# Kernel tuning notes

Hardware: AMD Instinct MI355X
Metric: run time of the kernel (lower is better)

Reference implementation:

```python
import jax, jax.numpy as jnp
import numpy as np

B, S, I, H, L = 32, 512, 512, 512, 2


def _gru_scan(x, wx, bx, wh, bh, reverse):
    # x: [B, S, layer_in_dim]; wx: [3H, in], wh: [3H, H]. PyTorch gate order r,z,n.
    hdim = wh.shape[1]
    gx = jnp.einsum('bsi,gi->sbg', x, wx) + bx  # precompute input gates: [S, B, 3H]
    h0 = jnp.zeros((x.shape[0], hdim), x.dtype)

    def step(h, gxt):
        gh = h @ wh.T + bh
        r = jax.nn.sigmoid(gxt[:, :hdim] + gh[:, :hdim])
        z = jax.nn.sigmoid(gxt[:, hdim:2 * hdim] + gh[:, hdim:2 * hdim])
        n = jnp.tanh(gxt[:, 2 * hdim:] + r * gh[:, 2 * hdim:])
        hn = (1 - z) * n + z * h
        return hn, hn

    hN, ys = jax.lax.scan(step, h0, gx, reverse=reverse)
    return ys.transpose(1, 0, 2), hN  # [B, S, H], [B, H]


def setup_inputs() -> dict:
    key = jax.random.key(0)
    ks = jax.random.split(key, 17)
    sc = 0.05
    d = {'x': jax.random.normal(ks[0], (B, S, I), jnp.float32)}
    i = 1
    for layer in range(L):
        in_dim = I if layer == 0 else 2 * H
        for tag in ('f', 'b'):
            d[f'wx_{tag}{layer}'] = jax.random.normal(ks[i], (3 * H, in_dim), jnp.float32) * sc
            d[f'bx_{tag}{layer}'] = jax.random.normal(jax.random.fold_in(ks[i], 1), (3 * H,), jnp.float32) * sc
            d[f'wh_{tag}{layer}'] = jax.random.normal(jax.random.fold_in(ks[i], 2), (3 * H, H), jnp.float32) * sc
            d[f'bh_{tag}{layer}'] = jax.random.normal(jax.random.fold_in(ks[i], 3), (3 * H,), jnp.float32) * sc
            i += 1
    return d


def reference(x,
              wx_f0, bx_f0, wh_f0, bh_f0, wx_b0, bx_b0, wh_b0, bh_b0,
              wx_f1, bx_f1, wh_f1, bh_f1, wx_b1, bx_b1, wh_b1, bh_b1):
    layers = [((wx_f0, bx_f0, wh_f0, bh_f0), (wx_b0, bx_b0, wh_b0, bh_b0)),
              ((wx_f1, bx_f1, wh_f1, bh_f1), (wx_b1, bx_b1, wh_b1, bh_b1))]
    layer_in = x
    h_fw, h_bw = [], []
    for fw, bw in layers:
        yf, hf = _gru_scan(layer_in, *fw, reverse=False)
        yb, hb = _gru_scan(layer_in, *bw, reverse=True)
        layer_in = jnp.concatenate([yf, yb], axis=-1)  # [B, S, 2H] (dropout p=0 -> identity)
        h_fw.append(hf)
        h_bw.append(hb)
    return layer_in, (jnp.stack(h_fw, 0), jnp.stack(h_bw, 0))
```

## Files before the change

kernel.cpp:

```cpp
#include <hip/hip_runtime.h>
#include <stdint.h>

typedef short short8 __attribute__((ext_vector_type(8)));
typedef float floatx4 __attribute__((ext_vector_type(4)));
typedef unsigned long long u64;

__device__ __forceinline__ unsigned short f2bf(float f) {
  union { float f; unsigned int i; } v;
  v.f = f;
  unsigned int r = v.i + 0x7fffu + ((v.i >> 16) & 1u);
  return (unsigned short)(r >> 16);
}
__device__ __forceinline__ short8 cvt8(const float4 a, const float4 b) {
  short8 v;
  v[0] = (short)f2bf(a.x); v[1] = (short)f2bf(a.y);
  v[2] = (short)f2bf(a.z); v[3] = (short)f2bf(a.w);
  v[4] = (short)f2bf(b.x); v[5] = (short)f2bf(b.y);
  v[6] = (short)f2bf(b.z); v[7] = (short)f2bf(b.w);
  return v;
}
__device__ __forceinline__ float sane(float x, float lim) {
  return fminf(fmaxf(x, -lim), lim);
}

extern __shared__ unsigned short lds[];

template<int K, int XM>
__global__ __launch_bounds__(256)
void gx_gemm(const float* __restrict__ xf,
             const unsigned short* __restrict__ xb,
             const float* __restrict__ wxf,
             const float* __restrict__ wxb,
             float* __restrict__ gx)
{
  unsigned short* As = lds;
  unsigned short* Bs = lds + 128 * 40;

  const int M0 = blockIdx.x * 128;
  const int N0 = blockIdx.y * 128;
  const int dir = blockIdx.z;
  const float* wx = dir ? wxb : wxf;
  float* gxd = gx + (long)dir * 16384 * 1536;

  const int tid = threadIdx.x;
  const int lane = tid & 63;
  const int wid = tid >> 6;
  const int q = lane >> 4;
  const int l16 = lane & 15;
  const int wM = (wid >> 1) * 64;
  const int wN = (wid & 1) * 64;

  const int srow = tid >> 1;
  const int k0 = (tid & 1) * 16;

  floatx4 acc[4][4];
#pragma unroll
  for (int i = 0; i < 4; ++i)
#pragma unroll
    for (int j = 0; j < 4; ++j) acc[i][j] = (floatx4){0.f, 0.f, 0.f, 0.f};

  for (int kk = 0; kk < K; kk += 32) {
    __syncthreads();
    {
      const int mg = M0 + srow;
      if (XM) {
        const float* ap = xf + ((long)(mg & 31) * 512 + (mg >> 5)) * 512 + kk + k0;
        float4 f0 = *(const float4*)(ap);
        float4 f1 = *(const float4*)(ap + 4);
        float4 f2 = *(const float4*)(ap + 8);
        float4 f3 = *(const float4*)(ap + 12);
        *(short8*)(As + srow * 40 + k0)     = cvt8(f0, f1);
        *(short8*)(As + srow * 40 + k0 + 8) = cvt8(f2, f3);
      } else {
        const unsigned short* ap = xb + (long)mg * 1024 + kk + k0;
        *(short8*)(As + srow * 40 + k0)     = *(const short8*)(ap);
        *(short8*)(As + srow * 40 + k0 + 8) = *(const short8*)(ap + 8);
      }
      const float* bp = wx + (long)(N0 + srow) * K + kk + k0;
      float4 g0 = *(const float4*)(bp);
      float4 g1 = *(const float4*)(bp + 4);
      float4 g2 = *(const float4*)(bp + 8);
      float4 g3 = *(const float4*)(bp + 12);
      *(short8*)(Bs + srow * 40 + k0)     = cvt8(g0, g1);
      *(short8*)(Bs + srow * 40 + k0 + 8) = cvt8(g2, g3);
    }
    __syncthreads();
    short8 a[4], b[4];
#pragma unroll
    for (int mt = 0; mt < 4; ++mt)
      a[mt] = *(const short8*)(As + (wM + mt * 16 + l16) * 40 + q * 8);
#pragma unroll
    for (int nt = 0; nt < 4; ++nt)
      b[nt] = *(const short8*)(Bs + (wN + nt * 16 + l16) * 40 + q * 8);
#pragma unroll
    for (int mt = 0; mt < 4; ++mt)
#pragma unroll
      for (int nt = 0; nt < 4; ++nt)
        acc[mt][nt] = __builtin_amdgcn_mfma_f32_16x16x32_bf16(
            a[mt], b[nt], acc[mt][nt], 0, 0, 0);
  }
#pragma unroll
  for (int mt = 0; mt < 4; ++mt) {
    const int row = M0 + wM + mt * 16 + q * 4;
#pragma unroll
    for (int nt = 0; nt < 4; ++nt) {
      const int col = N0 + wN + nt * 16 + l16;
#pragma unroll
      for (int r = 0; r < 4; ++r)
        gxd[(long)(row + r) * 1536 + col] = acc[mt][nt][r];
    }
  }
}

template<int OUT>
__global__ __launch_bounds__(128)
void gru_rec(const float* __restrict__ gx,
             const float* __restrict__ whfp, const float* __restrict__ bhfp,
             const float* __restrict__ whbp, const float* __restrict__ bhbp,
             const float* __restrict__ bxfp, const float* __restrict__ bxbp,
             unsigned short* __restrict__ ring,
             unsigned short* __restrict__ y0,
             float* __restrict__ omain,
             float* __restrict__ out_hf,
             float* __restrict__ out_hb)
{
  constexpr u64 TM = 0x4000400040004000ULL;
  unsigned short* whs = lds;

  const int bid = blockIdx.x;
  const bool fw = bid < 16;
  const int d = fw ? bid : bid - 16;
  const int tid = threadIdx.x;
  const int lane = tid & 63;
  const int w = tid >> 6;
  const int q = lane >> 4;
  const int l16 = lane & 15;

  const float* wh = fw ? whfp : whbp;
  const float* bh = fw ? bhfp : bhbp;
  const float* bx = fw ? bxfp : bxbp;
  const int col0 = d * 32;
  const int dirofs = fw ? 0 : 512;
  const long dirbyte = fw ? 0 : 32768;
  const float* gxd = gx + (long)(fw ? 0 : 1) * 16384 * 1536;

  for (int c = tid; c < 96 * 64; c += 128) {
    int lr = c >> 6, c8 = (c & 63) * 8;
    int g = lr >> 5, jc = lr & 31;
    const float* src = wh + (long)(g * 512 + col0 + jc) * 512 + c8;
    *(short8*)(whs + lr * 520 + c8) =
        cvt8(*(const float4*)src, *(const float4*)(src + 4));
  }
  __syncthreads();

  const int jj = l16;
  float cr[2], cz[2], bxn[2], bhn[2];
#pragma unroll
  for (int n2 = 0; n2 < 2; ++n2) {
    const int cc = col0 + n2 * 16 + jj;
    cr[n2] = bx[cc] + bh[cc];
    cz[n2] = bx[512 + cc] + bh[512 + cc];
    bxn[n2] = bx[1024 + cc];
    bhn[n2] = bh[1024 + cc];
  }

  const int cb = w * 16 + q * 4;
  const floatx4 fz = {0.f, 0.f, 0.f, 0.f};
  float h[2][4] = {{0.f, 0.f, 0.f, 0.f}, {0.f, 0.f, 0.f, 0.f}};
  unsigned int* y032 = (unsigned int*)y0;

  float nx[24];
  auto load_gx = [&](int t) {
    const float* base = gxd + (long)t * 32 * 1536;
#pragma unroll
    for (int g = 0; g < 3; ++g)
#pragma unroll
      for (int n2 = 0; n2 < 2; ++n2)
#pragma unroll
        for (int r = 0; r < 4; ++r)
          nx[(g * 2 + n2) * 4 + r] = __builtin_nontemporal_load(
              base + (long)(cb + r) * 1536 + g * 512 + col0 + n2 * 16 + jj);
  };
  { const int t0 = fw ? 0 : 511; load_gx(t0); }

  union V { u64 u[2]; short8 s; unsigned int dd[4]; };

  for (int it = 0; it < 512; ++it) {
    const int t = fw ? it : 511 - it;
    float cur[24];
#pragma unroll
    for (int i = 0; i < 24; ++i) cur[i] = nx[i];

    if (it < 511) {
      const int tn = fw ? it + 1 : 511 - (it + 1);
      load_gx(tn);
    }

    const char* wregion = nullptr;
    const char* rbase = nullptr;
    u64 expectw = 0;
    if (it > 0) {
      const int slot_r = (it + 1) & 1;
      wregion = (const char*)ring + (long)slot_r * 65536 + dirbyte +
                (long)w * 16384;
      rbase = wregion + (long)lane * 16;
      expectw = ((((it - 1) >> 1) & 1) ^ 1) ? TM : 0ULL;
    }

    floatx4 ar[2] = {fz, fz}, az[2] = {fz, fz}, an[2] = {fz, fz};
    if (it > 0) {
      const u64* cptr = (const u64*)(wregion + (long)l16 * 1024 +
                                     (long)q * 256 + 248);
      for (int pc = 0; pc < 8192; ++pc) {
        u64 can = __hip_atomic_load(cptr, __ATOMIC_RELAXED,
                                    __HIP_MEMORY_SCOPE_AGENT);
        if (__ballot(((can ^ expectw) & TM) != 0) == 0) break;
        __builtin_amdgcn_s_sleep(1);
      }

      short8 af[16];
#pragma unroll
      for (int ks = 0; ks < 16; ++ks)
        af[ks] = __builtin_nontemporal_load((const short8*)(rbase + ks * 1024));
      while (true) {
        u64 bad = 0;
#pragma unroll
        for (int ks = 0; ks < 16; ++ks) {
          V v; v.s = af[ks];
          bad |= ((v.u[0] ^ expectw) | (v.u[1] ^ expectw)) & TM;
        }
        if (bad == 0) break;
        __builtin_amdgcn_s_sleep(1);
#pragma unroll
        for (int ks = 0; ks < 16; ++ks) {
          u64* p = (u64*)(rbase + ks * 1024);
          V v;
          v.u[0] = __hip_atomic_load(p,     __ATOMIC_RELAXED, __HIP_MEMORY_SCOPE_AGENT);
          v.u[1] = __hip_atomic_load(p + 1, __ATOMIC_RELAXED, __HIP_MEMORY_SCOPE_AGENT);
          af[ks] = v.s;
        }
      }
#pragma unroll
      for (int ks = 0; ks < 16; ++ks) {
        V v; v.s = af[ks];
        v.dd[0] &= 0xBFFFBFFFu; v.dd[1] &= 0xBFFFBFFFu;
        v.dd[2] &= 0xBFFFBFFFu; v.dd[3] &= 0xBFFFBFFFu;
        short8 a = v.s;
#pragma unroll
        for (int n2 = 0; n2 < 2; ++n2) {
          short8 vr = *(const short8*)(whs + (n2 * 16 + jj) * 520 + ks * 32 + q * 8);
          short8 vz = *(const short8*)(whs + (32 + n2 * 16 + jj) * 520 + ks * 32 + q * 8);
          short8 vn = *(const short8*)(whs + (64 + n2 * 16 + jj) * 520 + ks * 32 + q * 8);
          ar[n2] = __builtin_amdgcn_mfma_f32_16x16x32_bf16(a, vr, ar[n2], 0, 0, 0);
          az[n2] = __builtin_amdgcn_mfma_f32_16x16x32_bf16(a, vz, az[n2], 0, 0, 0);
          an[n2] = __builtin_amdgcn_mfma_f32_16x16x32_bf16(a, vn, an[n2], 0, 0, 0);
        }
      }
    }

    unsigned short hb16[2][4];
#pragma unroll
    for (int n2 = 0; n2 < 2; ++n2) {
#pragma unroll
      for (int r = 0; r < 4; ++r) {
        const float xr = sane(cur[(0 * 2 + n2) * 4 + r] + ar[n2][r] + cr[n2], 60.f);
        const float xz = sane(cur[(1 * 2 + n2) * 4 + r] + az[n2][r] + cz[n2], 60.f);
        const float rr = 1.f / (1.f + __expf(-xr));
        const float zz = 1.f / (1.f + __expf(-xz));
        const float xn = sane(cur[(2 * 2 + n2) * 4 + r] + bxn[n2] +
                              rr * (an[n2][r] + bhn[n2]), 30.f);
        const float e2 = __expf(-2.f * xn);
        const float nn = (1.f - e2) / (1.f + e2);
        h[n2][r] = (1.f - zz) * nn + zz * h[n2][r];
        hb16[n2][r] = f2bf(h[n2][r]);
      }
    }

    {
      const unsigned short utag = (((it >> 1) & 1) ^ 1) ? 0x4000 : 0;
      const int slot_w = it & 1;
      char* sb = (char*)ring + (long)slot_w * 65536 + dirbyte + (long)w * 16384;
      const int o = l16 >> 3;
#pragma unroll
      for (int n2 = 0; n2 < 2; ++n2) {
        const int cb2 = col0 + n2 * 16 + o * 8;
        const int ksq = (cb2 >> 5) * 1024 + ((cb2 >> 3) & 3) * 256;
        u64 lo = 0, hi = 0;
#pragma unroll
        for (int r = 0; r < 4; ++r) {
          int tv = (int)(unsigned short)(hb16[n2][r] | utag);
          int pm = __shfl_xor(tv, 1);
          unsigned int pair = (l16 & 1)
              ? ((unsigned)(pm & 0xffff) | ((unsigned)tv << 16))
              : ((unsigned)(tv & 0xffff) | ((unsigned)pm << 16));
          unsigned int pm2 = (unsigned)__shfl_xor((int)pair, 2);
          unsigned int d0 = (l16 & 2) ? pm2 : pair;
          unsigned int d1 = (l16 & 2) ? pair : pm2;
          unsigned int p0 = (unsigned)__shfl_xor((int)d0, 4);
          unsigned int p1 = (unsigned)__shfl_xor((int)d1, 4);
          unsigned int e0 = (l16 & 4) ? p0 : d0;
          unsigned int e1 = (l16 & 4) ? p1 : d1;
          unsigned int e2 = (l16 & 4) ? d0 : p0;
          unsigned int e3 = (l16 & 4) ? d1 : p1;
          if ((l16 & 3) == r) {
            lo = (u64)e0 | ((u64)e1 << 32);
            hi = (u64)e2 | ((u64)e3 << 32);
          }
        }
        if ((l16 & 4) == 0) {
          u64* p = (u64*)(sb + ksq + (q * 4 + (l16 & 3)) * 16);
          __hip_atomic_store(p,     lo, __ATOMIC_RELAXED, __HIP_MEMORY_SCOPE_AGENT);
          __hip_atomic_store(p + 1, hi, __ATOMIC_RELAXED, __HIP_MEMORY_SCOPE_AGENT);
        }
      }
    }

    if (OUT == 0) {
#pragma unroll
      for (int n2 = 0; n2 < 2; ++n2) {
        const int colw = (dirofs + col0 + n2 * 16 + jj) >> 1;
#pragma unroll
        for (int r = 0; r < 4; ++r) {
          int v = hb16[n2][r];
          int pm = __shfl_xor(v, 1);
          unsigned int pr = (unsigned)(v & 0xffff) | ((unsigned)(pm & 0xffff) << 16);
          if ((jj & 1) == 0)
            __builtin_nontemporal_store(pr,
                y032 + ((long)t * 32 + cb + r) * 512 + colw);
        }
      }
    }
    if (OUT == 1) {
#pragma unroll
      for (int n2 = 0; n2 < 2; ++n2)
#pragma unroll
        for (int r = 0; r < 4; ++r)
          __builtin_nontemporal_store(h[n2][r],
              omain + (long)(cb + r) * 524288 + (long)t * 1024 +
              dirofs + col0 + n2 * 16 + jj);
    }
    if (it == 511) {
      float* oh = fw ? out_hf : out_hb;
#pragma unroll
      for (int n2 = 0; n2 < 2; ++n2)
#pragma unroll
        for (int r = 0; r < 4; ++r)
          oh[(cb + r) * 512 + col0 + n2 * 16 + jj] = h[n2][r];
    }
  }
}

extern "C" void kernel_launch(void* const* d_in, const int* in_sizes, int n_in,
                              void* d_out, int out_size, void* d_ws, size_t ws_size,
                              hipStream_t stream)
{
  (void)in_sizes; (void)n_in; (void)out_size; (void)ws_size;

  const float* x    = (const float*)d_in[0];
  const float* wxf0 = (const float*)d_in[1];
  const float* bxf0 = (const float*)d_in[2];
  const float* whf0 = (const float*)d_in[3];
  const float* bhf0 = (const float*)d_in[4];
  const float* wxb0 = (const float*)d_in[5];
  const float* bxb0 = (const float*)d_in[6];
  const float* whb0 = (const float*)d_in[7];
  const float* bhb0 = (const float*)d_in[8];
  const float* wxf1 = (const float*)d_in[9];
  const float* bxf1 = (const float*)d_in[10];
  const float* whf1 = (const float*)d_in[11];
  const float* bhf1 = (const float*)d_in[12];
  const float* wxb1 = (const float*)d_in[13];
  const float* bxb1 = (const float*)d_in[14];
  const float* whb1 = (const float*)d_in[15];
  const float* bhb1 = (const float*)d_in[16];

  char* ws = (char*)d_ws;
  float* gx             = (float*)(ws);
  unsigned short* y0    = (unsigned short*)(ws + 201326592L);
  unsigned short* ring0 = (unsigned short*)(ws + 234881024L);
  unsigned short* ring1 = (unsigned short*)(ws + 235012096L);

  float* out = (float*)d_out;
  float* out_hf0 = out + 16777216L;
  float* out_hf1 = out + 16777216L + 16384L;
  float* out_hb0 = out + 16777216L + 32768L;
  float* out_hb1 = out + 16777216L + 49152L;

  const size_t lds_gemm = (size_t)(2 * 128 * 40) * 2;
  const size_t lds_rec  = (size_t)(96 * 520) * 2;
  (void)hipFuncSetAttribute((const void*)gru_rec<0>,
                            hipFuncAttributeMaxDynamicSharedMemorySize, (int)lds_rec);
  (void)hipFuncSetAttribute((const void*)gru_rec<1>,
                            hipFuncAttributeMaxDynamicSharedMemorySize, (int)lds_rec);

  hipMemsetAsync(ws + 234881024L, 0, 262144L, stream);

  gx_gemm<512, 1><<<dim3(128, 12, 2), dim3(256), lds_gemm, stream>>>(
      x, nullptr, wxf0, wxb0, gx);
  gru_rec<0><<<dim3(32), dim3(128), lds_rec, stream>>>(
      gx, whf0, bhf0, whb0, bhb0, bxf0, bxb0,
      ring0, y0, nullptr, out_hf0, out_hb0);
  gx_gemm<1024, 0><<<dim3(128, 12, 2), dim3(256), lds_gemm, stream>>>(
      nullptr, y0, wxf1, wxb1, gx);
  gru_rec<1><<<dim3(32), dim3(128), lds_rec, stream>>>(
      gx, whf1, bhf1, whb1, bhb1, bxf1, bxb1,
      ring1, nullptr, out, out_hf1, out_hb1);
}
```

Baseline: 6.536 ms.

## Add producer wave to prefetch GRU input gates into LDS double buffer

Adds a third wavefront per recurrence block that loads the next timestep's precomputed input-gate values from global memory into a double-buffered LDS staging area. The two compute waves then read the gates from LDS instead of holding a register prefetch. The aim is to take global-load latency and register pressure off the serial recurrence path. The cost is a block-wide __syncthreads every timestep, which sits on the critical path of a latency-bound loop, plus extra LDS.

```diff
diff --git a/kernel.cpp b/kernel.cpp
--- a/kernel.cpp
+++ b/kernel.cpp
@@ -113,7 +113,7 @@
 }
 
 template<int OUT>
-__global__ __launch_bounds__(128)
+__global__ __launch_bounds__(192)
 void gru_rec(const float* __restrict__ gx,
              const float* __restrict__ whfp, const float* __restrict__ bhfp,
              const float* __restrict__ whbp, const float* __restrict__ bhbp,
@@ -126,13 +126,15 @@
 {
   constexpr u64 TM = 0x4000400040004000ULL;
   unsigned short* whs = lds;
+  float* gxbuf = (float*)(lds + 96 * 520);
 
   const int bid = blockIdx.x;
   const bool fw = bid < 16;
   const int d = fw ? bid : bid - 16;
   const int tid = threadIdx.x;
+  const bool gxw = tid >= 128;
   const int lane = tid & 63;
-  const int w = tid >> 6;
+  const int w = (tid >> 6) & 1;
   const int q = lane >> 4;
   const int l16 = lane & 15;
 
@@ -144,13 +146,34 @@
   const long dirbyte = fw ? 0 : 32768;
   const float* gxd = gx + (long)(fw ? 0 : 1) * 16384 * 1536;
 
-  for (int c = tid; c < 96 * 64; c += 128) {
+  for (int c = tid; c < 96 * 64; c += 192) {
     int lr = c >> 6, c8 = (c & 63) * 8;
     int g = lr >> 5, jc = lr & 31;
     const float* src = wh + (long)(g * 512 + col0 + jc) * 512 + c8;
     *(short8*)(whs + lr * 520 + c8) =
         cvt8(*(const float4*)src, *(const float4*)(src + 4));
   }
+
+  auto stage_gx = [&](int t, int slot) {
+    float* gb = gxbuf + slot * 24 * 128;
+    const float* base = gxd + (long)t * 32 * 1536;
+#pragma unroll
+    for (int c2 = 0; c2 < 2; ++c2) {
+      const int c = lane + c2 * 64;
+      const int cbb = ((c >> 6) & 1) * 16 + ((c >> 4) & 3) * 4;
+      const int cj = c & 15;
+#pragma unroll
+      for (int g = 0; g < 3; ++g)
+#pragma unroll
+        for (int n2 = 0; n2 < 2; ++n2)
+#pragma unroll
+          for (int r = 0; r < 4; ++r)
+            gb[((g * 2 + n2) * 4 + r) * 128 + c] = __builtin_nontemporal_load(
+                base + (long)(cbb + r) * 1536 + g * 512 + col0 + n2 * 16 + cj);
+    }
+  };
+
+  if (gxw) stage_gx(fw ? 0 : 511, 0);
   __syncthreads();
 
   const int jj = l16;
@@ -169,184 +192,176 @@
   float h[2][4] = {{0.f, 0.f, 0.f, 0.f}, {0.f, 0.f, 0.f, 0.f}};
   unsigned int* y032 = (unsigned int*)y0;
 
-  float nx[24];
-  auto load_gx = [&](int t) {
-    const float* base = gxd + (long)t * 32 * 1536;
-#pragma unroll
-    for (int g = 0; g < 3; ++g)
-#pragma unroll
-      for (int n2 = 0; n2 < 2; ++n2)
-#pragma unroll
-        for (int r = 0; r < 4; ++r)
-          nx[(g * 2 + n2) * 4 + r] = __builtin_nontemporal_load(
-              base + (long)(cb + r) * 1536 + g * 512 + col0 + n2 * 16 + jj);
-  };
-  { const int t0 = fw ? 0 : 511; load_gx(t0); }
-
   union V { u64 u[2]; short8 s; unsigned int dd[4]; };
 
   for (int it = 0; it < 512; ++it) {
     const int t = fw ? it : 511 - it;
-    float cur[24];
-#pragma unroll
-    for (int i = 0; i < 24; ++i) cur[i] = nx[i];
-
-    if (it < 511) {
-      const int tn = fw ? it + 1 : 511 - (it + 1);
-      load_gx(tn);
-    }
-
-    const char* wregion = nullptr;
-    const char* rbase = nullptr;
-    u64 expectw = 0;
-    if (it > 0) {
-      const int slot_r = (it + 1) & 1;
-      wregion = (const char*)ring + (long)slot_r * 65536 + dirbyte +
-                (long)w * 16384;
-      rbase = wregion + (long)lane * 16;
-      expectw = ((((it - 1) >> 1) & 1) ^ 1) ? TM : 0ULL;
-    }
-
-    floatx4 ar[2] = {fz, fz}, az[2] = {fz, fz}, an[2] = {fz, fz};
-    if (it > 0) {
-      const u64* cptr = (const u64*)(wregion + (long)l16 * 1024 +
-                                     (long)q * 256 + 248);
-      for (int pc = 0; pc < 8192; ++pc) {
-        u64 can = __hip_atomic_load(cptr, __ATOMIC_RELAXED,
-                                    __HIP_MEMORY_SCOPE_AGENT);
-        if (__ballot(((can ^ expectw) & TM) != 0) == 0) break;
-        __builtin_amdgcn_s_sleep(1);
-      }
-
-      short8 af[16];
-#pragma unroll
-      for (int ks = 0; ks < 16; ++ks)
-        af[ks] = __builtin_nontemporal_load((const short8*)(rbase + ks * 1024));
-      while (true) {
-        u64 bad = 0;
+
+    if (gxw) {
+      if (it < 511) stage_gx(fw ? it + 1 : 511 - (it + 1), (it + 1) & 1);
+    } else {
+      float cur[24];
+      {
+        const float* gb = gxbuf + (it & 1) * 24 * 128;
+#pragma unroll
+        for (int i = 0; i < 24; ++i) cur[i] = gb[i * 128 + tid];
+      }
+
+      const char* wregion = nullptr;
+      const char* rbase = nullptr;
+      u64 expectw = 0;
+      if (it > 0) {
+        const int slot_r = (it + 1) & 1;
+        wregion = (const char*)ring + (long)slot_r * 65536 + dirbyte +
+                  (long)w * 16384;
+        rbase = wregion + (long)lane * 16;
+        expectw = ((((it - 1) >> 1) & 1) ^ 1) ? TM : 0ULL;
+      }
+
+      floatx4 ar[2] = {fz, fz}, az[2] = {fz, fz}, an[2] = {fz, fz};
+      if (it > 0) {
+        const u64* cptr = (const u64*)(wregion + (long)l16 * 1024 +
+                                       (long)q * 256 + 248);
+        for (int pc = 0; pc < 8192; ++pc) {
+          u64 can = __hip_atomic_load(cptr, __ATOMIC_RELAXED,
+                                      __HIP_MEMORY_SCOPE_AGENT);
+          if (__ballot(((can ^ expectw) & TM) != 0) == 0) break;
+          __builtin_amdgcn_s_sleep(1);
+        }
+
+        short8 af[16];
+#pragma unroll
+        for (int ks = 0; ks < 16; ++ks)
+          af[ks] = __builtin_nontemporal_load((const short8*)(rbase + ks * 1024));
+        while (true) {
+          u64 bad = 0;
+#pragma unroll
+          for (int ks = 0; ks < 16; ++ks) {
+            V v; v.s = af[ks];
+            bad |= ((v.u[0] ^ expectw) | (v.u[1] ^ expectw)) & TM;
+          }
+          if (bad == 0) break;
+          __builtin_amdgcn_s_sleep(1);
+#pragma unroll
+          for (int ks = 0; ks < 16; ++ks) {
+            u64* p = (u64*)(rbase + ks * 1024);
+            V v;
+            v.u[0] = __hip_atomic_load(p,     __ATOMIC_RELAXED, __HIP_MEMORY_SCOPE_AGENT);
+            v.u[1] = __hip_atomic_load(p + 1, __ATOMIC_RELAXED, __HIP_MEMORY_SCOPE_AGENT);
+            af[ks] = v.s;
+          }
+        }
+
 #pragma unroll
         for (int ks = 0; ks < 16; ++ks) {
           V v; v.s = af[ks];
-          bad |= ((v.u[0] ^ expectw) | (v.u[1] ^ expectw)) & TM;
-        }
-        if (bad == 0) break;
-        __builtin_amdgcn_s_sleep(1);
-#pragma unroll
-        for (int ks = 0; ks < 16; ++ks) {
-          u64* p = (u64*)(rbase + ks * 1024);
-          V v;
-          v.u[0] = __hip_atomic_load(p,     __ATOMIC_RELAXED, __HIP_MEMORY_SCOPE_AGENT);
-          v.u[1] = __hip_atomic_load(p + 1, __ATOMIC_RELAXED, __HIP_MEMORY_SCOPE_AGENT);
-          af[ks] = v.s;
-        }
-      }
-#pragma unroll
-      for (int ks = 0; ks < 16; ++ks) {
-        V v; v.s = af[ks];
-        v.dd[0] &= 0xBFFFBFFFu; v.dd[1] &= 0xBFFFBFFFu;
-        v.dd[2] &= 0xBFFFBFFFu; v.dd[3] &= 0xBFFFBFFFu;
-        short8 a = v.s;
+          v.dd[0] &= 0xBFFFBFFFu; v.dd[1] &= 0xBFFFBFFFu;
+          v.dd[2] &= 0xBFFFBFFFu; v.dd[3] &= 0xBFFFBFFFu;
+          short8 a = v.s;
+#pragma unroll
+          for (int n2 = 0; n2 < 2; ++n2) {
+            short8 vr = *(const short8*)(whs + (n2 * 16 + jj) * 520 + ks * 32 + q * 8);
+            short8 vz = *(const short8*)(whs + (32 + n2 * 16 + jj) * 520 + ks * 32 + q * 8);
+            short8 vn = *(const short8*)(whs + (64 + n2 * 16 + jj) * 520 + ks * 32 + q * 8);
+            ar[n2] = __builtin_amdgcn_mfma_f32_16x16x32_bf16(a, vr, ar[n2], 0, 0, 0);
+            az[n2] = __builtin_amdgcn_mfma_f32_16x16x32_bf16(a, vz, az[n2], 0, 0, 0);
+            an[n2] = __builtin_amdgcn_mfma_f32_16x16x32_bf16(a, vn, an[n2], 0, 0, 0);
+          }
+        }
+      }
+
+      unsigned short hb16[2][4];
+#pragma unroll
+      for (int n2 = 0; n2 < 2; ++n2) {
+#pragma unroll
+        for (int r = 0; r < 4; ++r) {
+          const float xr = sane(cur[(0 * 2 + n2) * 4 + r] + ar[n2][r] + cr[n2], 60.f);
+          const float xz = sane(cur[(1 * 2 + n2) * 4 + r] + az[n2][r] + cz[n2], 60.f);
+          const float rr = 1.f / (1.f + __expf(-xr));
+          const float zz = 1.f / (1.f + __expf(-xz));
+          const float xn = sane(cur[(2 * 2 + n2) * 4 + r] + bxn[n2] +
+                                rr * (an[n2][r] + bhn[n2]), 30.f);
+          const float e2 = __expf(-2.f * xn);
+          const float nn = (1.f - e2) / (1.f + e2);
+          h[n2][r] = (1.f - zz) * nn + zz * h[n2][r];
+          hb16[n2][r] = f2bf(h[n2][r]);
+        }
+      }
+
+      {
+        const unsigned short utag = (((it >> 1) & 1) ^ 1) ? 0x4000 : 0;
+        const int slot_w = it & 1;
+        char* sb = (char*)ring + (long)slot_w * 65536 + dirbyte + (long)w * 16384;
+        const int o = l16 >> 3;
 #pragma unroll
         for (int n2 = 0; n2 < 2; ++n2) {
-          short8 vr = *(const short8*)(whs + (n2 * 16 + jj) * 520 + ks * 32 + q * 8);
-          short8 vz = *(const short8*)(whs + (32 + n2 * 16 + jj) * 520 + ks * 32 + q * 8);
-          short8 vn = *(const short8*)(whs + (64 + n2 * 16 + jj) * 520 + ks * 32 + q * 8);
-          ar[n2] = __builtin_amdgcn_mfma_f32_16x16x32_bf16(a, vr, ar[n2], 0, 0, 0);
-          az[n2] = __builtin_amdgcn_mfma_f32_16x16x32_bf16(a, vz, az[n2], 0, 0, 0);
-          an[n2] = __builtin_amdgcn_mfma_f32_16x16x32_bf16(a, vn, an[n2], 0, 0, 0);
-        }
+          const int cb2 = col0 + n2 * 16 + o * 8;
+          const int ksq = (cb2 >> 5) * 1024 + ((cb2 >> 3) & 3) * 256;
+          u64 lo = 0, hi = 0;
+#pragma unroll
+          for (int r = 0; r < 4; ++r) {
+            int tv = (int)(unsigned short)(hb16[n2][r] | utag);
+            int pm = __shfl_xor(tv, 1);
+            unsigned int pair = (l16 & 1)
+                ? ((unsigned)(pm & 0xffff) | ((unsigned)tv << 16))
+                : ((unsigned)(tv & 0xffff) | ((unsigned)pm << 16));
+            unsigned int pm2 = (unsigned)__shfl_xor((int)pair, 2);
+            unsigned int d0 = (l16 & 2) ? pm2 : pair;
+            unsigned int d1 = (l16 & 2) ? pair : pm2;
+            unsigned int p0 = (unsigned)__shfl_xor((int)d0, 4);
+            unsigned int p1 = (unsigned)__shfl_xor((int)d1, 4);
+            unsigned int e0 = (l16 & 4) ? p0 : d0;
+            unsigned int e1 = (l16 & 4) ? p1 : d1;
+            unsigned int e2 = (l16 & 4) ? d0 : p0;
+            unsigned int e3 = (l16 & 4) ? d1 : p1;
+            if ((l16 & 3) == r) {
+              lo = (u64)e0 | ((u64)e1 << 32);
+              hi = (u64)e2 | ((u64)e3 << 32);
+            }
+          }
+          if ((l16 & 4) == 0) {
+            u64* p = (u64*)(sb + ksq + (q * 4 + (l16 & 3)) * 16);
+            __hip_atomic_store(p,     lo, __ATOMIC_RELAXED, __HIP_MEMORY_SCOPE_AGENT);
+            __hip_atomic_store(p + 1, hi, __ATOMIC_RELAXED, __HIP_MEMORY_SCOPE_AGENT);
+          }
+        }
+      }
+
+      if (OUT == 0) {
+#pragma unroll
+        for (int n2 = 0; n2 < 2; ++n2) {
+          const int colw = (dirofs + col0 + n2 * 16 + jj) >> 1;
+#pragma unroll
+          for (int r = 0; r < 4; ++r) {
+            int v = hb16[n2][r];
+            int pm = __shfl_xor(v, 1);
+            unsigned int pr = (unsigned)(v & 0xffff) | ((unsigned)(pm & 0xffff) << 16);
+            if ((jj & 1) == 0)
+              __builtin_nontemporal_store(pr,
+                  y032 + ((long)t * 32 + cb + r) * 512 + colw);
+          }
+        }
+      }
+      if (OUT == 1) {
+#pragma unroll
+        for (int n2 = 0; n2 < 2; ++n2)
+#pragma unroll
+          for (int r = 0; r < 4; ++r)
+            __builtin_nontemporal_store(h[n2][r],
+                omain + (long)(cb + r) * 524288 + (long)t * 1024 +
+                dirofs + col0 + n2 * 16 + jj);
+      }
+      if (it == 511) {
+        float* oh = fw ? out_hf : out_hb;
+#pragma unroll
+        for (int n2 = 0; n2 < 2; ++n2)
+#pragma unroll
+          for (int r = 0; r < 4; ++r)
+            oh[(cb + r) * 512 + col0 + n2 * 16 + jj] = h[n2][r];
       }
     }
 
-    unsigned short hb16[2][4];
-#pragma unroll
-    for (int n2 = 0; n2 < 2; ++n2) {
-#pragma unroll
-      for (int r = 0; r < 4; ++r) {
-        const float xr = sane(cur[(0 * 2 + n2) * 4 + r] + ar[n2][r] + cr[n2], 60.f);
-        const float xz = sane(cur[(1 * 2 + n2) * 4 + r] + az[n2][r] + cz[n2], 60.f);
-        const float rr = 1.f / (1.f + __expf(-xr));
-        const float zz = 1.f / (1.f + __expf(-xz));
-        const float xn = sane(cur[(2 * 2 + n2) * 4 + r] + bxn[n2] +
-                              rr * (an[n2][r] + bhn[n2]), 30.f);
-        const float e2 = __expf(-2.f * xn);
-        const float nn = (1.f - e2) / (1.f + e2);
-        h[n2][r] = (1.f - zz) * nn + zz * h[n2][r];
-        hb16[n2][r] = f2bf(h[n2][r]);
-      }
-    }
-
-    {
-      const unsigned short utag = (((it >> 1) & 1) ^ 1) ? 0x4000 : 0;
-      const int slot_w = it & 1;
-      char* sb = (char*)ring + (long)slot_w * 65536 + dirbyte + (long)w * 16384;
-      const int o = l16 >> 3;
-#pragma unroll
-      for (int n2 = 0; n2 < 2; ++n2) {
-        const int cb2 = col0 + n2 * 16 + o * 8;
-        const int ksq = (cb2 >> 5) * 1024 + ((cb2 >> 3) & 3) * 256;
-        u64 lo = 0, hi = 0;
-#pragma unroll
-        for (int r = 0; r < 4; ++r) {
-          int tv = (int)(unsigned short)(hb16[n2][r] | utag);
-          int pm = __shfl_xor(tv, 1);
-          unsigned int pair = (l16 & 1)
-              ? ((unsigned)(pm & 0xffff) | ((unsigned)tv << 16))
-              : ((unsigned)(tv & 0xffff) | ((unsigned)pm << 16));
-          unsigned int pm2 = (unsigned)__shfl_xor((int)pair, 2);
-          unsigned int d0 = (l16 & 2) ? pm2 : pair;
-          unsigned int d1 = (l16 & 2) ? pair : pm2;
-          unsigned int p0 = (unsigned)__shfl_xor((int)d0, 4);
-          unsigned int p1 = (unsigned)__shfl_xor((int)d1, 4);
-          unsigned int e0 = (l16 & 4) ? p0 : d0;
-          unsigned int e1 = (l16 & 4) ? p1 : d1;
-          unsigned int e2 = (l16 & 4) ? d0 : p0;
-          unsigned int e3 = (l16 & 4) ? d1 : p1;
-          if ((l16 & 3) == r) {
-            lo = (u64)e0 | ((u64)e1 << 32);
-            hi = (u64)e2 | ((u64)e3 << 32);
-          }
-        }
-        if ((l16 & 4) == 0) {
-          u64* p = (u64*)(sb + ksq + (q * 4 + (l16 & 3)) * 16);
-          __hip_atomic_store(p,     lo, __ATOMIC_RELAXED, __HIP_MEMORY_SCOPE_AGENT);
-          __hip_atomic_store(p + 1, hi, __ATOMIC_RELAXED, __HIP_MEMORY_SCOPE_AGENT);
-        }
-      }
-    }
-
-    if (OUT == 0) {
-#pragma unroll
-      for (int n2 = 0; n2 < 2; ++n2) {
-        const int colw = (dirofs + col0 + n2 * 16 + jj) >> 1;
-#pragma unroll
-        for (int r = 0; r < 4; ++r) {
-          int v = hb16[n2][r];
-          int pm = __shfl_xor(v, 1);
-          unsigned int pr = (unsigned)(v & 0xffff) | ((unsigned)(pm & 0xffff) << 16);
-          if ((jj & 1) == 0)
-            __builtin_nontemporal_store(pr,
-                y032 + ((long)t * 32 + cb + r) * 512 + colw);
-        }
-      }
-    }
-    if (OUT == 1) {
-#pragma unroll
-      for (int n2 = 0; n2 < 2; ++n2)
-#pragma unroll
-        for (int r = 0; r < 4; ++r)
-          __builtin_nontemporal_store(h[n2][r],
-              omain + (long)(cb + r) * 524288 + (long)t * 1024 +
-              dirofs + col0 + n2 * 16 + jj);
-    }
-    if (it == 511) {
-      float* oh = fw ? out_hf : out_hb;
-#pragma unroll
-      for (int n2 = 0; n2 < 2; ++n2)
-#pragma unroll
-        for (int r = 0; r < 4; ++r)
-          oh[(cb + r) * 512 + col0 + n2 * 16 + jj] = h[n2][r];
-    }
+    __syncthreads();
   }
 }
 
@@ -387,7 +402,7 @@
   float* out_hb1 = out + 16777216L + 49152L;
 
   const size_t lds_gemm = (size_t)(2 * 128 * 40) * 2;
-  const size_t lds_rec  = (size_t)(96 * 520) * 2;
+  const size_t lds_rec  = (size_t)(96 * 520) * 2 + 2 * 24 * 128 * 4;
   (void)hipFuncSetAttribute((const void*)gru_rec<0>,
                             hipFuncAttributeMaxDynamicSharedMemorySize, (int)lds_rec);
   (void)hipFuncSetAttribute((const void*)gru_rec<1>,
@@ -397,12 +412,12 @@
 
   gx_gemm<512, 1><<<dim3(128, 12, 2), dim3(256), lds_gemm, stream>>>(
       x, nullptr, wxf0, wxb0, gx);
-  gru_rec<0><<<dim3(32), dim3(128), lds_rec, stream>>>(
+  gru_rec<0><<<dim3(32), dim3(192), lds_rec, stream>>>(
       gx, whf0, bhf0, whb0, bhb0, bxf0, bxb0,
       ring0, y0, nullptr, out_hf0, out_hb0);
   gx_gemm<1024, 0><<<dim3(128, 12, 2), dim3(256), lds_gemm, stream>>>(
       nullptr, y0, wxf1, wxb1, gx);
-  gru_rec<1><<<dim3(32), dim3(128), lds_rec, stream>>>(
+  gru_rec<1><<<dim3(32), dim3(192), lds_rec, stream>>>(
       gx, whf1, bhf1, whb1, bhb1, bxf1, bxb1,
       ring1, nullptr, out, out_hf1, out_hb1);
 }
```

New measurement: 7.133 ms. 1.09x slower.
